# Performance work log

Measured on AMD Instinct MI355X. Metric: run time of the kernel, lower is better.

Reference implementation:

```python
import jax, jax.numpy as jnp
import numpy as np

N, E, F_IN, HID, H1, H2, H3, OUT = 10000, 160000, 50, 350, 4, 4, 6, 121


def _gat(x, src, dst, n, W, a_s, a_d, b, heads, C, concat):
    # PyG GATConv (dropout=0, eval): h = xW^T reshaped to [N,H,C]
    h = (x @ W.T).reshape(n, heads, C)
    alpha_src = jnp.einsum('nhc,hc->nh', h, a_s)  # [N,H]
    alpha_dst = jnp.einsum('nhc,hc->nh', h, a_d)  # [N,H]
    e = jax.nn.leaky_relu(alpha_src[src] + alpha_dst[dst], 0.2)  # [E,H]
    # numerically-stable segment softmax over incoming edges of each dst node
    m = jax.ops.segment_max(e, dst, num_segments=n)
    ee = jnp.exp(e - m[dst])
    s = jax.ops.segment_sum(ee, dst, num_segments=n)
    alpha = ee / s[dst]  # self-loops guarantee s > 0
    out = jax.ops.segment_sum(h[src] * alpha[:, :, None], dst, num_segments=n)  # [N,H,C]
    out = out.reshape(n, heads * C) if concat else out.mean(axis=1)
    return out + b


def setup_inputs() -> dict:
    key = jax.random.key(0)
    ks = jax.random.split(key, 16)
    sc = 0.05
    inp = {
        'x': jax.random.normal(ks[0], (N, F_IN), dtype=jnp.float32),
        'edge_index': jax.random.randint(ks[1], (2, E), 0, N, dtype=jnp.int64) if jax.config.jax_enable_x64 else jax.random.randint(ks[1], (2, E), 0, N, dtype=jnp.int32),
        'W1': jax.random.normal(ks[2], (H1 * HID, F_IN), dtype=jnp.float32) * sc,
        'a1s': jax.random.normal(ks[3], (H1, HID), dtype=jnp.float32) * sc,
        'a1d': jax.random.normal(ks[4], (H1, HID), dtype=jnp.float32) * sc,
        'b1': jnp.zeros((H1 * HID,), dtype=jnp.float32),
        'W2': jax.random.normal(ks[5], (H2 * HID, H1 * HID), dtype=jnp.float32) * sc,
        'a2s': jax.random.normal(ks[6], (H2, HID), dtype=jnp.float32) * sc,
        'a2d': jax.random.normal(ks[7], (H2, HID), dtype=jnp.float32) * sc,
        'b2': jnp.zeros((H2 * HID,), dtype=jnp.float32),
        'Wskip': jax.random.normal(ks[8], (H2 * HID, H1 * HID), dtype=jnp.float32) * sc,
        'W3': jax.random.normal(ks[9], (H3 * OUT, H2 * HID), dtype=jnp.float32) * sc,
        'a3s': jax.random.normal(ks[10], (H3, OUT), dtype=jnp.float32) * sc,
        'a3d': jax.random.normal(ks[11], (H3, OUT), dtype=jnp.float32) * sc,
        'b3': jnp.zeros((OUT,), dtype=jnp.float32),
    }
    return inp


def reference(x, edge_index, W1, a1s, a1d, b1, W2, a2s, a2d, b2, Wskip, W3, a3s, a3d, b3):
    n = x.shape[0]
    loops = jnp.arange(n, dtype=edge_index.dtype)  # PyG add_self_loops=True
    src = jnp.concatenate([edge_index[0], loops])
    dst = jnp.concatenate([edge_index[1], loops])
    h = jax.nn.elu(_gat(x, src, dst, n, W1, a1s, a1d, b1, H1, HID, True))
    x_in = h
    h = jax.nn.elu(_gat(h, src, dst, n, W2, a2s, a2d, b2, H2, HID, True))
    h = h + x_in @ Wskip.T  # skip connection (bias=False)
    return _gat(h, src, dst, n, W3, a3s, a3d, b3, H3, OUT, False)
```

## Files before the change

### kernel.cpp

```cpp
#include <hip/hip_runtime.h>
#include <math.h>

#define NNODES 10000
#define NEDGES 160000
#define E2 (NEDGES + NNODES)
#define F_IN 50
#define HIDC 350
#define NH1 4
#define NH2 4
#define NH3 6
#define OUTC 121
#define MAXE 96
#define KP1 64
#define KP2 1408
#define LD3 736
#define ROWSLACK 128

typedef __attribute__((ext_vector_type(8))) short short8;
typedef __attribute__((ext_vector_type(8))) unsigned short ushort8v;
typedef __attribute__((ext_vector_type(4))) float floatx4;

static __device__ __forceinline__ unsigned short f2bf(float f) {
    unsigned u = __float_as_uint(f);
    unsigned r = (u + 0x7fffu + ((u >> 16) & 1u)) >> 16;
    return (unsigned short)r;
}
static __device__ __forceinline__ float bf2f(unsigned short s) {
    return __uint_as_float(((unsigned)s) << 16);
}

#define GLL16(gp, lp)                                                      \
    __builtin_amdgcn_global_load_lds(                                      \
        (const __attribute__((address_space(1))) void*)(gp),               \
        (__attribute__((address_space(3))) void*)(lp), 16, 0, 0)

__global__ void count_kernel(const int* __restrict__ ei, int* __restrict__ cnt) {
    int i = blockIdx.x * blockDim.x + threadIdx.x;
    if (i >= E2) return;
    int dst = (i < NEDGES) ? ei[NEDGES + i] : (i - NEDGES);
    atomicAdd(&cnt[dst], 1);
}

__global__ void scan_kernel(const int* __restrict__ cnt, int* __restrict__ indptr,
                            int* __restrict__ cursor) {
    __shared__ int part[1024];
    int tid = threadIdx.x;
    const int CH = (NNODES + 1023) / 1024;
    int base = tid * CH;
    int s = 0;
    for (int i = 0; i < CH; i++) {
        int idx = base + i;
        if (idx < NNODES) s += cnt[idx];
    }
    part[tid] = s;
    __syncthreads();
    for (int off = 1; off < 1024; off <<= 1) {
        int v = (tid >= off) ? part[tid - off] : 0;
        __syncthreads();
        part[tid] += v;
        __syncthreads();
    }
    int run = (tid == 0) ? 0 : part[tid - 1];
    for (int i = 0; i < CH; i++) {
        int idx = base + i;
        if (idx < NNODES) {
            indptr[idx] = run;
            cursor[idx] = run;
            run += cnt[idx];
        }
    }
    if (tid == 0) indptr[NNODES] = part[1023];
}

__global__ void scatter_kernel(const int* __restrict__ ei, int* __restrict__ cursor,
                               int* __restrict__ esrc) {
    int i = blockIdx.x * blockDim.x + threadIdx.x;
    if (i >= E2) return;
    int src, dst;
    if (i < NEDGES) {
        src = ei[i];
        dst = ei[NEDGES + i];
    } else {
        src = dst = i - NEDGES;
    }
    int pos = atomicAdd(&cursor[dst], 1);
    esrc[pos] = src;
}

__global__ void splitW1_kernel(const float* __restrict__ W1,
                               unsigned short* __restrict__ w1Hi,
                               unsigned short* __restrict__ w1Lo) {
    int k = threadIdx.x;
    int r = blockIdx.x;
    float v = (k < F_IN) ? W1[(size_t)r * F_IN + k] : 0.f;
    unsigned short h = f2bf(v);
    w1Hi[(size_t)r * KP1 + k] = h;
    w1Lo[(size_t)r * KP1 + k] = f2bf(v - bf2f(h));
}

__global__ void splitB_kernel(const float* __restrict__ W2, const float* __restrict__ Wsk,
                              const float* __restrict__ W3,
                              unsigned short* __restrict__ w2Hi,
                              unsigned short* __restrict__ w3Hi) {
    int k = blockIdx.x * blockDim.x + threadIdx.x;
    if (k >= KP2) return;
    int r = blockIdx.y;
    const int K = 1400;
    const float* src;
    unsigned short* hi;
    int row;
    if (r < 1400) { src = W2; row = r; hi = w2Hi; }
    else if (r < 2800) { src = Wsk; row = r - 1400; hi = w2Hi + (size_t)1400 * KP2; }
    else { src = W3; row = r - 2800; hi = w3Hi; }
    float v = (k < K) ? src[(size_t)row * K + k] : 0.f;
    hi[(size_t)row * KP2 + k] = f2bf(v);
}

__global__ void atil_kernel(const float* __restrict__ W, const float* __restrict__ av_s,
                            const float* __restrict__ av_d, float* __restrict__ outS,
                            float* __restrict__ outD, int C, int K, int cchunk) {
    int k = blockIdx.x * 64 + (threadIdx.x & 63);
    if (k >= K) return;
    int h = blockIdx.y;
    int c0 = blockIdx.z * cchunk;
    int c1 = c0 + cchunk;
    if (c1 > C) c1 = C;
    float ss = 0.f, dd = 0.f;
    for (int c = c0; c < c1; c++) {
        float wv = W[((size_t)h * C + c) * K + k];
        ss = fmaf(wv, av_s[h * C + c], ss);
        dd = fmaf(wv, av_d[h * C + c], dd);
    }
    atomicAdd(&outS[(size_t)h * K + k], ss);
    atomicAdd(&outD[(size_t)h * K + k], dd);
}

__global__ __launch_bounds__(256) void alpha1x_kernel(const float* __restrict__ x,
                                                      const float* __restrict__ at1s,
                                                      const float* __restrict__ at1d,
                                                      float* __restrict__ as1,
                                                      float* __restrict__ ad1) {
    int wave = threadIdx.x >> 6, lane = threadIdx.x & 63;
    int n = blockIdx.x * 4 + wave;
    if (n >= NNODES) return;
    int kk = lane < F_IN ? lane : F_IN - 1;
    float v = (lane < F_IN) ? x[(size_t)n * F_IN + lane] : 0.f;
    float p[8];
#pragma unroll
    for (int h = 0; h < 4; h++) {
        p[h] = v * at1s[h * F_IN + kk];
        p[4 + h] = v * at1d[h * F_IN + kk];
    }
#pragma unroll
    for (int s = 0; s < 8; s++)
#pragma unroll
        for (int o = 32; o > 0; o >>= 1) p[s] += __shfl_xor(p[s], o, 64);
    if (lane == 0) {
#pragma unroll
        for (int h = 0; h < 4; h++) {
            as1[n * 4 + h] = p[h];
            ad1[n * 4 + h] = p[4 + h];
        }
    }
}

__global__ void zeropad_kernel(unsigned short* __restrict__ hi) {
    int i = blockIdx.x * 256 + threadIdx.x;
    if (i >= NNODES * 8) return;
    int n = i >> 3, c = 1400 + (i & 7);
    hi[(size_t)n * KP2 + c] = 0;
}

__global__ __launch_bounds__(256) void agg_x(
    const float* __restrict__ x, const float* __restrict__ as_n,
    const float* __restrict__ ad_n, const int* __restrict__ indptr,
    const int* __restrict__ esrc, unsigned short* __restrict__ xaggHi,
    unsigned short* __restrict__ xaggLo) {
    int n = blockIdx.x, tid = threadIdx.x;
    int s = indptr[n], e = indptr[n + 1];
    int deg = e - s;
    if (deg > MAXE) deg = MAXE;
    __shared__ int srcs[MAXE];
    __shared__ float wgt[MAXE * 4];

    if (tid < 64) {
        int lane = tid;
        float adv[4], mx[4], sm[4];
#pragma unroll
        for (int h = 0; h < 4; h++) {
            adv[h] = ad_n[n * 4 + h];
            mx[h] = -1e30f;
            sm[h] = 0.f;
        }
        for (int j = lane; j < deg; j += 64) {
            int sr = esrc[s + j];
            srcs[j] = sr;
#pragma unroll
            for (int h = 0; h < 4; h++) {
                float ev = as_n[sr * 4 + h] + adv[h];
                ev = ev > 0.f ? ev : 0.2f * ev;
                wgt[j * 4 + h] = ev;
                mx[h] = fmaxf(mx[h], ev);
            }
        }
#pragma unroll
        for (int h = 0; h < 4; h++)
#pragma unroll
            for (int o = 32; o > 0; o >>= 1) mx[h] = fmaxf(mx[h], __shfl_xor(mx[h], o, 64));
        for (int j = lane; j < deg; j += 64) {
#pragma unroll
            for (int h = 0; h < 4; h++) {
                float p = __expf(wgt[j * 4 + h] - mx[h]);
                wgt[j * 4 + h] = p;
                sm[h] += p;
            }
        }
#pragma unroll
        for (int h = 0; h < 4; h++) {
#pragma unroll
            for (int o = 32; o > 0; o >>= 1) sm[h] += __shfl_xor(sm[h], o, 64);
            sm[h] = 1.f / sm[h];
        }
        for (int j = lane; j < deg; j += 64) {
#pragma unroll
            for (int h = 0; h < 4; h++) wgt[j * 4 + h] *= sm[h];
        }
    }
    __syncthreads();

    int h = tid >> 6, k = tid & 63;
    float a = 0.f;
    if (k < F_IN) {
        float a2 = 0.f;
        int j = 0;
        for (; j + 1 < deg; j += 2) {
            a = fmaf(wgt[j * 4 + h], x[(size_t)srcs[j] * F_IN + k], a);
            a2 = fmaf(wgt[(j + 1) * 4 + h], x[(size_t)srcs[j + 1] * F_IN + k], a2);
        }
        if (j < deg) a = fmaf(wgt[j * 4 + h], x[(size_t)srcs[j] * F_IN + k], a);
        a += a2;
    }
    unsigned short hi = f2bf(a);
    xaggHi[(size_t)n * 256 + tid] = hi;
    xaggLo[(size_t)n * 256 + tid] = f2bf(a - bf2f(hi));
}

__global__ __launch_bounds__(256, 2) void gemm_h1(
    const unsigned short* __restrict__ xaggHi, const unsigned short* __restrict__ xaggLo,
    const unsigned short* __restrict__ w1Hi, const unsigned short* __restrict__ w1Lo,
    const float* __restrict__ bias, unsigned short* __restrict__ actHi) {
    __shared__ __align__(16) unsigned short sA[2][128 * 32];
    __shared__ __align__(16) unsigned short sB[2][256 * 32];
    int tid = threadIdx.x;
    int wave = tid >> 6, lane = tid & 63;
    int wm = (wave >> 1) * 64, wn = (wave & 1) * 128;
    int fr = lane & 15, kq = lane >> 4;
    int row0 = blockIdx.y * 128, col0 = blockIdx.x * 256;
    int hd = blockIdx.z;

    floatx4 acc[4][8];
#pragma unroll
    for (int i = 0; i < 4; i++)
#pragma unroll
        for (int j = 0; j < 8; j++)
#pragma unroll
            for (int q = 0; q < 4; q++) acc[i][j][q] = 0.f;

    int gpos = lane & 3;
    int rl = lane >> 2;
    int gsw = kq ^ ((fr >> 1) & 3);

    for (int k0 = 0; k0 < 64; k0 += 32) {
#pragma unroll
        for (int c = 0; c < 2; ++c) {
            int r = wave * 32 + c * 16 + rl;
            int g = gpos ^ ((r >> 1) & 3);
            size_t gofs = (size_t)(row0 + r) * 256 + hd * 64 + k0 + g * 8;
            size_t lofs = (size_t)r * 32 + (size_t)gpos * 8;
            GLL16(xaggHi + gofs, &sA[0][lofs]);
            GLL16(xaggLo + gofs, &sA[1][lofs]);
        }
#pragma unroll
        for (int c = 0; c < 4; ++c) {
            int r = wave * 64 + c * 16 + rl;
            int g = gpos ^ ((r >> 1) & 3);
            size_t gofs = (size_t)(hd * 350 + col0 + r) * KP1 + k0 + g * 8;
            size_t lofs = (size_t)r * 32 + (size_t)gpos * 8;
            GLL16(w1Hi + gofs, &sB[0][lofs]);
            GLL16(w1Lo + gofs, &sB[1][lofs]);
        }
        __syncthreads();

        short8 ah[4], al[4], bh[8], bl[8];
#pragma unroll
        for (int j = 0; j < 8; j++) {
            int rb = wn + j * 16 + fr;
            bh[j] = *(const short8*)&sB[0][rb * 32 + gsw * 8];
            bl[j] = *(const short8*)&sB[1][rb * 32 + gsw * 8];
        }
#pragma unroll
        for (int i = 0; i < 4; i++) {
            int ra = wm + i * 16 + fr;
            ah[i] = *(const short8*)&sA[0][ra * 32 + gsw * 8];
            al[i] = *(const short8*)&sA[1][ra * 32 + gsw * 8];
        }
#pragma unroll
        for (int i = 0; i < 4; i++)
#pragma unroll
            for (int j = 0; j < 8; j++) {
                acc[i][j] = __builtin_amdgcn_mfma_f32_16x16x32_bf16(ah[i], bh[j],
                                                                   acc[i][j], 0, 0, 0);
                acc[i][j] = __builtin_amdgcn_mfma_f32_16x16x32_bf16(al[i], bh[j],
                                                                   acc[i][j], 0, 0, 0);
                acc[i][j] = __builtin_amdgcn_mfma_f32_16x16x32_bf16(ah[i], bl[j],
                                                                   acc[i][j], 0, 0, 0);
            }
        __syncthreads();
    }

#pragma unroll
    for (int i = 0; i < 4; i++) {
#pragma unroll
        for (int rg = 0; rg < 4; rg++) {
            int rr = row0 + wm + i * 16 + kq * 4 + rg;
            if (rr >= NNODES) continue;
#pragma unroll
            for (int j = 0; j < 8; j++) {
                int cc = col0 + wn + j * 16 + fr;
                if (cc < 350) {
                    int gc = hd * 350 + cc;
                    float v = acc[i][j][rg] + bias[gc];
                    v = v > 0.f ? v : expm1f(v);
                    actHi[(size_t)rr * KP2 + gc] = f2bf(v);
                }
            }
        }
    }
}

__global__ __launch_bounds__(256) void alpha_act(
    const unsigned short* __restrict__ actHi, const float* __restrict__ ats,
    const float* __restrict__ atd, float* __restrict__ asx, float* __restrict__ adx) {
    int wave = threadIdx.x >> 6, lane = threadIdx.x & 63;
    int n = blockIdx.x * 4 + wave;
    if (n >= NNODES) return;
    float p[8] = {0.f, 0.f, 0.f, 0.f, 0.f, 0.f, 0.f, 0.f};
    for (int u = lane; u < 175; u += 64) {
        int cb = u * 8;
        const ushort8v v8 = *(const ushort8v*)(actHi + (size_t)n * KP2 + cb);
#pragma unroll
        for (int q = 0; q < 8; q++) {
            float v = bf2f(v8[q]);
#pragma unroll
            for (int h = 0; h < 4; h++) {
                p[h] = fmaf(v, ats[h * 1400 + cb + q], p[h]);
                p[4 + h] = fmaf(v, atd[h * 1400 + cb + q], p[4 + h]);
            }
        }
    }
#pragma unroll
    for (int q = 0; q < 8; q++)
#pragma unroll
        for (int o = 32; o > 0; o >>= 1) p[q] += __shfl_xor(p[q], o, 64);
    if (lane == 0) {
#pragma unroll
        for (int h = 0; h < 4; h++) {
            asx[n * 4 + h] = p[h];
            adx[n * 4 + h] = p[4 + h];
        }
    }
}

__global__ __launch_bounds__(256, 2) void gemm_b16(
    const unsigned short* __restrict__ A, const unsigned short* __restrict__ B,
    unsigned short* __restrict__ Cb, int NN, int M, int Kp, int ldc) {
    __shared__ __align__(16) unsigned short sA[128 * 32];
    __shared__ __align__(16) unsigned short sB[256 * 32];
    int tid = threadIdx.x;
    int wave = tid >> 6, lane = tid & 63;
    int wm = (wave >> 1) * 64, wn = (wave & 1) * 128;
    int fr = lane & 15, kq = lane >> 4;
    int row0 = blockIdx.y * 128, col0 = blockIdx.x * 256;

    floatx4 acc[4][8];
#pragma unroll
    for (int i = 0; i < 4; i++)
#pragma unroll
        for (int j = 0; j < 8; j++)
#pragma unroll
            for (int q = 0; q < 4; q++) acc[i][j][q] = 0.f;

    int gpos = lane & 3;
    int rl = lane >> 2;
    int gsw = kq ^ ((fr >> 1) & 3);

    for (int k0 = 0; k0 < Kp; k0 += 32) {
#pragma unroll
        for (int c = 0; c < 2; ++c) {
            int r = wave * 32 + c * 16 + rl;
            int g = gpos ^ ((r >> 1) & 3);
            GLL16(A + (size_t)(row0 + r) * Kp + k0 + g * 8,
                  &sA[(size_t)r * 32 + (size_t)gpos * 8]);
        }
#pragma unroll
        for (int c = 0; c < 4; ++c) {
            int r = wave * 64 + c * 16 + rl;
            int g = gpos ^ ((r >> 1) & 3);
            GLL16(B + (size_t)(col0 + r) * Kp + k0 + g * 8,
                  &sB[(size_t)r * 32 + (size_t)gpos * 8]);
        }
        __syncthreads();

        short8 ah[4], bh[8];
#pragma unroll
        for (int j = 0; j < 8; j++) {
            int rb = wn + j * 16 + fr;
            bh[j] = *(const short8*)&sB[rb * 32 + gsw * 8];
        }
#pragma unroll
        for (int i = 0; i < 4; i++) {
            int ra = wm + i * 16 + fr;
            ah[i] = *(const short8*)&sA[ra * 32 + gsw * 8];
        }
#pragma unroll
        for (int i = 0; i < 4; i++)
#pragma unroll
            for (int j = 0; j < 8; j++)
                acc[i][j] = __builtin_amdgcn_mfma_f32_16x16x32_bf16(ah[i], bh[j],
                                                                   acc[i][j], 0, 0, 0);
        __syncthreads();
    }

#pragma unroll
    for (int i = 0; i < 4; i++) {
#pragma unroll
        for (int rg = 0; rg < 4; rg++) {
            int rr = row0 + wm + i * 16 + kq * 4 + rg;
            if (rr >= NN) continue;
#pragma unroll
            for (int j = 0; j < 8; j++) {
                int cc = col0 + wn + j * 16 + fr;
                if (cc < M) Cb[(size_t)rr * ldc + cc] = f2bf(acc[i][j][rg]);
            }
        }
    }
}

#define AGG_T 192
template <int H, int C, int MODE, int DOELU, int SKIP, int HN>
__global__ __launch_bounds__(AGG_T) void agg2(
    const unsigned short* __restrict__ hpreb, int ldh,
    const float* __restrict__ as_n, const float* __restrict__ ad_n,
    const int* __restrict__ indptr, const int* __restrict__ esrc,
    const float* __restrict__ bias, unsigned short* __restrict__ outHi, int Kp,
    float* __restrict__ outF, const float* __restrict__ atns,
    const float* __restrict__ atnd, float* __restrict__ asx,
    float* __restrict__ adx) {
    constexpr int HC = H * C;
    int n = blockIdx.x;
    int tid = threadIdx.x;
    int s = indptr[n], e = indptr[n + 1];
    int deg = e - s;
    if (deg > MAXE) deg = MAXE;

    __shared__ int srcs[MAXE];
    __shared__ float wgt[MAXE * H];
    __shared__ float aggsh[MODE ? HC : 1];
    __shared__ float sAl[16];
    if (tid < 16) sAl[tid] = 0.f;

    if (tid < 64) {
        int lane = tid;
        float adv[H], mx[H], sm[H];
#pragma unroll
        for (int h = 0; h < H; h++) {
            adv[h] = ad_n[n * H + h];
            mx[h] = -1e30f;
            sm[h] = 0.f;
        }
        for (int j = lane; j < deg; j += 64) {
            int sr = esrc[s + j];
            srcs[j] = sr;
#pragma unroll
            for (int h = 0; h < H; h++) {
                float ev = as_n[sr * H + h] + adv[h];
                ev = ev > 0.f ? ev : 0.2f * ev;
                wgt[j * H + h] = ev;
                mx[h] = fmaxf(mx[h], ev);
            }
        }
#pragma unroll
        for (int h = 0; h < H; h++)
#pragma unroll
            for (int o = 32; o > 0; o >>= 1) mx[h] = fmaxf(mx[h], __shfl_xor(mx[h], o, 64));
        for (int j = lane; j < deg; j += 64) {
#pragma unroll
            for (int h = 0; h < H; h++) {
                float p = __expf(wgt[j * H + h] - mx[h]);
                wgt[j * H + h] = p;
                sm[h] += p;
            }
        }
#pragma unroll
        for (int h = 0; h < H; h++) {
#pragma unroll
            for (int o = 32; o > 0; o >>= 1) sm[h] += __shfl_xor(sm[h], o, 64);
            sm[h] = 1.f / sm[h];
        }
        for (int j = lane; j < deg; j += 64) {
#pragma unroll
            for (int h = 0; h < H; h++) wgt[j * H + h] *= sm[h];
        }
    }
    __syncthreads();

    if (MODE == 0) {
        constexpr int NV8 = HC / 8;
        constexpr int NP = (HN > 0) ? 2 * HN : 1;
        float p[NP];
#pragma unroll
        for (int q = 0; q < NP; q++) p[q] = 0.f;

        for (int c8 = tid; c8 < NV8; c8 += AGG_T) {
            int cb = c8 * 8;
            int hh[8];
#pragma unroll
            for (int q = 0; q < 8; q++) hh[q] = (cb + q) / C;
            float av[8];
#pragma unroll
            for (int q = 0; q < 8; q++) av[q] = 0.f;
            int j = 0;
            for (; j + 3 < deg; j += 4) {
                const ushort8v v0 = *(const ushort8v*)(hpreb + (size_t)srcs[j] * ldh + cb);
                const ushort8v v1 = *(const ushort8v*)(hpreb + (size_t)srcs[j + 1] * ldh + cb);
                const ushort8v v2 = *(const ushort8v*)(hpreb + (size_t)srcs[j + 2] * ldh + cb);
                const ushort8v v3 = *(const ushort8v*)(hpreb + (size_t)srcs[j + 3] * ldh + cb);
                const float* w0 = &wgt[j * H];
                const float* w1 = &wgt[(j + 1) * H];
                const float* w2 = &wgt[(j + 2) * H];
                const float* w3 = &wgt[(j + 3) * H];
#pragma unroll
                for (int q = 0; q < 8; q++) av[q] = fmaf(w0[hh[q]], bf2f(v0[q]), av[q]);
#pragma unroll
                for (int q = 0; q < 8; q++) av[q] = fmaf(w1[hh[q]], bf2f(v1[q]), av[q]);
#pragma unroll
                for (int q = 0; q < 8; q++) av[q] = fmaf(w2[hh[q]], bf2f(v2[q]), av[q]);
#pragma unroll
                for (int q = 0; q < 8; q++) av[q] = fmaf(w3[hh[q]], bf2f(v3[q]), av[q]);
            }
            for (; j < deg; j++) {
                const ushort8v v0 = *(const ushort8v*)(hpreb + (size_t)srcs[j] * ldh + cb);
                const float* w0 = &wgt[j * H];
#pragma unroll
                for (int q = 0; q < 8; q++) av[q] = fmaf(w0[hh[q]], bf2f(v0[q]), av[q]);
            }
#pragma unroll
            for (int q = 0; q < 8; q++) av[q] += bias[cb + q];
            if (DOELU) {
#pragma unroll
                for (int q = 0; q < 8; q++) av[q] = av[q] > 0.f ? av[q] : expm1f(av[q]);
            }
            if (SKIP) {
                const ushort8v sk = *(const ushort8v*)(hpreb + (size_t)n * ldh + 1400 + cb);
#pragma unroll
                for (int q = 0; q < 8; q++) av[q] += bf2f(sk[q]);
            }
            if (HN > 0) {
#pragma unroll
                for (int h = 0; h < HN; h++) {
                    float ss = 0.f, dd = 0.f;
#pragma unroll
                    for (int q = 0; q < 8; q++) {
                        ss = fmaf(av[q], atns[(size_t)h * HC + cb + q], ss);
                        dd = fmaf(av[q], atnd[(size_t)h * HC + cb + q], dd);
                    }
                    p[h] += ss;
                    p[HN + h] += dd;
                }
            }
            ushort8v hi8;
#pragma unroll
            for (int q = 0; q < 8; q++) hi8[q] = f2bf(av[q]);
            *(ushort8v*)(outHi + (size_t)n * Kp + cb) = hi8;
        }
        for (int c = HC + tid; c < Kp; c += AGG_T) outHi[(size_t)n * Kp + c] = 0;
        if (HN > 0) {
#pragma unroll
            for (int q = 0; q < NP; q++)
#pragma unroll
                for (int o = 32; o > 0; o >>= 1) p[q] += __shfl_xor(p[q], o, 64);
            if ((tid & 63) == 0) {
#pragma unroll
                for (int q = 0; q < NP; q++) atomicAdd(&sAl[q], p[q]);
            }
            __syncthreads();
            if (tid < HN) asx[n * HN + tid] = sAl[tid];
            else if (tid < 2 * HN) adx[n * HN + (tid - HN)] = sAl[tid];
        }
    } else {
        constexpr int NV8 = (HC + 7) / 8;
        for (int c8 = tid; c8 < NV8; c8 += AGG_T) {
            int cb = c8 * 8;
            int hh[8];
#pragma unroll
            for (int q = 0; q < 8; q++) {
                int cc = cb + q;
                hh[q] = (cc < HC) ? cc / C : (H - 1);
            }
            float av[8];
#pragma unroll
            for (int q = 0; q < 8; q++) av[q] = 0.f;
            int j = 0;
            for (; j + 3 < deg; j += 4) {
                const ushort8v v0 = *(const ushort8v*)(hpreb + (size_t)srcs[j] * ldh + cb);
                const ushort8v v1 = *(const ushort8v*)(hpreb + (size_t)srcs[j + 1] * ldh + cb);
                const ushort8v v2 = *(const ushort8v*)(hpreb + (size_t)srcs[j + 2] * ldh + cb);
                const ushort8v v3 = *(const ushort8v*)(hpreb + (size_t)srcs[j + 3] * ldh + cb);
                const float* w0 = &wgt[j * H];
                const float* w1 = &wgt[(j + 1) * H];
                const float* w2 = &wgt[(j + 2) * H];
                const float* w3 = &wgt[(j + 3) * H];
#pragma unroll
                for (int q = 0; q < 8; q++) av[q] = fmaf(w0[hh[q]], bf2f(v0[q]), av[q]);
#pragma unroll
                for (int q = 0; q < 8; q++) av[q] = fmaf(w1[hh[q]], bf2f(v1[q]), av[q]);
#pragma unroll
                for (int q = 0; q < 8; q++) av[q] = fmaf(w2[hh[q]], bf2f(v2[q]), av[q]);
#pragma unroll
                for (int q = 0; q < 8; q++) av[q] = fmaf(w3[hh[q]], bf2f(v3[q]), av[q]);
            }
            for (; j < deg; j++) {
                const ushort8v v0 = *(const ushort8v*)(hpreb + (size_t)srcs[j] * ldh + cb);
                const float* w0 = &wgt[j * H];
#pragma unroll
                for (int q = 0; q < 8; q++) av[q] = fmaf(w0[hh[q]], bf2f(v0[q]), av[q]);
            }
#pragma unroll
            for (int q = 0; q < 8; q++)
                if (cb + q < HC) aggsh[cb + q] = av[q];
        }
        __syncthreads();
        for (int c = tid; c < C; c += AGG_T) {
            float sres = 0.f;
#pragma unroll
            for (int h = 0; h < H; h++) sres += aggsh[h * C + c];
            outF[(size_t)n * C + c] = sres * (1.f / (float)H) + bias[c];
        }
    }
}

extern "C" void kernel_launch(void* const* d_in, const int* in_sizes, int n_in,
                              void* d_out, int out_size, void* d_ws, size_t ws_size,
                              hipStream_t stream) {
    const float* x = (const float*)d_in[0];
    const int* ei = (const int*)d_in[1];
    const float* W1 = (const float*)d_in[2];
    const float* a1s = (const float*)d_in[3];
    const float* a1d = (const float*)d_in[4];
    const float* b1 = (const float*)d_in[5];
    const float* W2 = (const float*)d_in[6];
    const float* a2s = (const float*)d_in[7];
    const float* a2d = (const float*)d_in[8];
    const float* b2 = (const float*)d_in[9];
    const float* Wsk = (const float*)d_in[10];
    const float* W3 = (const float*)d_in[11];
    const float* a3s = (const float*)d_in[12];
    const float* a3d = (const float*)d_in[13];
    const float* b3 = (const float*)d_in[14];
    float* out = (float*)d_out;

    char* w = (char*)d_ws;
    size_t off = 0;
    auto alloc = [&](size_t bytes) -> char* {
        char* p = w + off;
        off += (bytes + 255) & ~(size_t)255;
        return p;
    };
    unsigned short* hpreb = (unsigned short*)alloc((size_t)(NNODES + ROWSLACK) * 2800 * 2);
    unsigned short* actHi = (unsigned short*)alloc((size_t)(NNODES + ROWSLACK) * KP2 * 2);
    unsigned short* xaggHi = (unsigned short*)alloc((size_t)(NNODES + ROWSLACK) * 256 * 2);
    unsigned short* xaggLo = (unsigned short*)alloc((size_t)(NNODES + ROWSLACK) * 256 * 2);
    unsigned short* w1Hi = (unsigned short*)alloc((size_t)(1400 + 512) * KP1 * 2);
    unsigned short* w1Lo = (unsigned short*)alloc((size_t)(1400 + 512) * KP1 * 2);
    unsigned short* w2Hi = (unsigned short*)alloc((size_t)(2800 + ROWSLACK) * KP2 * 2);
    unsigned short* w3Hi = (unsigned short*)alloc((size_t)(726 + ROWSLACK) * KP2 * 2);
    float* atall = (float*)alloc((size_t)28400 * 4);
    int* cnt = (int*)alloc((size_t)(NNODES + 16) * 4);
    float* at1s = atall;
    float* at1d = atall + 200;
    float* at2s = atall + 400;
    float* at2d = atall + 6000;
    float* at3s = atall + 11600;
    float* at3d = atall + 20000;
    float* asP = (float*)alloc((size_t)NNODES * 6 * 4);
    float* adP = (float*)alloc((size_t)NNODES * 6 * 4);
    float* asQ = (float*)alloc((size_t)NNODES * 6 * 4);
    float* adQ = (float*)alloc((size_t)NNODES * 6 * 4);
    int* indptr = (int*)alloc((size_t)(NNODES + 16) * 4);
    int* cursor = (int*)alloc((size_t)(NNODES + 16) * 4);
    int* esrc = (int*)alloc((size_t)E2 * 4);

    size_t zbytes = (size_t)((char*)cnt - (char*)atall) + (NNODES + 16) * 4;
    hipMemsetAsync(atall, 0, zbytes, stream);

    splitW1_kernel<<<1400, 64, 0, stream>>>(W1, w1Hi, w1Lo);
    splitB_kernel<<<dim3(6, 2800 + 726), 256, 0, stream>>>(W2, Wsk, W3, w2Hi, w3Hi);
    atil_kernel<<<dim3(1, 4, 5), 64, 0, stream>>>(W1, a1s, a1d, at1s, at1d, HIDC, F_IN, 70);
    atil_kernel<<<dim3(22, 4, 5), 64, 0, stream>>>(W2, a2s, a2d, at2s, at2d, HIDC, 1400, 70);
    atil_kernel<<<dim3(22, 6, 4), 64, 0, stream>>>(W3, a3s, a3d, at3s, at3d, OUTC, 1400, 31);
    alpha1x_kernel<<<(NNODES + 3) / 4, 256, 0, stream>>>(x, at1s, at1d, asP, adP);

    count_kernel<<<(E2 + 255) / 256, 256, 0, stream>>>(ei, cnt);
    scan_kernel<<<1, 1024, 0, stream>>>(cnt, indptr, cursor);
    scatter_kernel<<<(E2 + 255) / 256, 256, 0, stream>>>(ei, cursor, esrc);

    zeropad_kernel<<<(NNODES * 8 + 255) / 256, 256, 0, stream>>>(actHi);

    dim3 blk(256);
    int gy = (NNODES + 127) / 128;

    agg_x<<<NNODES, 256, 0, stream>>>(x, asP, adP, indptr, esrc, xaggHi, xaggLo);
    gemm_h1<<<dim3(2, gy, 4), blk, 0, stream>>>(xaggHi, xaggLo, w1Hi, w1Lo, b1, actHi);
    alpha_act<<<(NNODES + 3) / 4, 256, 0, stream>>>(actHi, at2s, at2d, asQ, adQ);

    {
        int M = 2800;
        dim3 grid((M + 255) / 256, gy);
        gemm_b16<<<grid, blk, 0, stream>>>(actHi, w2Hi, hpreb, NNODES, M, KP2, 2800);
        agg2<NH2, HIDC, 0, 1, 1, 6><<<NNODES, AGG_T, 0, stream>>>(
            hpreb, 2800, asQ, adQ, indptr, esrc, b2, actHi, KP2, nullptr,
            at3s, at3d, asP, adP);
    }
    {
        int M = NH3 * OUTC;
        dim3 grid((M + 255) / 256, gy);
        gemm_b16<<<grid, blk, 0, stream>>>(actHi, w3Hi, hpreb, NNODES, M, KP2, LD3);
        agg2<NH3, OUTC, 1, 0, 0, 0><<<NNODES, AGG_T, 0, stream>>>(
            hpreb, LD3, asP, adP, indptr, esrc, b3, nullptr, 0, out,
            nullptr, nullptr, nullptr, nullptr);
    }
}
```

Before: 632.3 us.

## Compute layer-2 attention logits with MFMA and simplify head-weight selection in aggregation

Replaces the scalar per-node dot-product kernel that computes layer-2 attention logits with an MFMA kernel. Each wave handles 16 nodes against a 16-row bf16 hi/lo split of the folded attention vectors, and a new small kernel prepares that split. Separately, the aggregation kernels stop computing a per-element head index with integer division. Instead they pick between two preloaded per-edge weights based on a split point, which cuts LDS loads and divides in the inner edge loop. The MFMA path adds a setup kernel and relies on the padded activation columns being zero.

After: 635.1 us. No clear change (+0.4%).

```diff
diff --git a/kernel.cpp b/kernel.cpp
--- a/kernel.cpp
+++ b/kernel.cpp
@@ -135,6 +135,21 @@
     atomicAdd(&outD[(size_t)h * K + k], dd);
 }
 
+__global__ void splitAT2_kernel(const float* __restrict__ atall,
+                                unsigned short* __restrict__ atHi,
+                                unsigned short* __restrict__ atLo) {
+    int k = blockIdx.x * 64 + threadIdx.x;
+    int r = blockIdx.y;
+    float v = 0.f;
+    if (k < 1400) {
+        if (r < 4) v = atall[400 + r * 1400 + k];
+        else if (r < 8) v = atall[6000 + (r - 4) * 1400 + k];
+    }
+    unsigned short h = f2bf(v);
+    atHi[(size_t)r * KP2 + k] = h;
+    atLo[(size_t)r * KP2 + k] = f2bf(v - bf2f(h));
+}
+
 __global__ __launch_bounds__(256) void alpha1x_kernel(const float* __restrict__ x,
                                                       const float* __restrict__ at1s,
                                                       const float* __restrict__ at1d,
@@ -338,36 +353,31 @@
     }
 }
 
-__global__ __launch_bounds__(256) void alpha_act(
-    const unsigned short* __restrict__ actHi, const float* __restrict__ ats,
-    const float* __restrict__ atd, float* __restrict__ asx, float* __restrict__ adx) {
+__global__ __launch_bounds__(256) void alpha_mfma(
+    const unsigned short* __restrict__ act, const unsigned short* __restrict__ tHi,
+    const unsigned short* __restrict__ tLo, int H, float* __restrict__ asx,
+    float* __restrict__ adx) {
     int wave = threadIdx.x >> 6, lane = threadIdx.x & 63;
-    int n = blockIdx.x * 4 + wave;
-    if (n >= NNODES) return;
-    float p[8] = {0.f, 0.f, 0.f, 0.f, 0.f, 0.f, 0.f, 0.f};
-    for (int u = lane; u < 175; u += 64) {
-        int cb = u * 8;
-        const ushort8v v8 = *(const ushort8v*)(actHi + (size_t)n * KP2 + cb);
-#pragma unroll
-        for (int q = 0; q < 8; q++) {
-            float v = bf2f(v8[q]);
-#pragma unroll
-            for (int h = 0; h < 4; h++) {
-                p[h] = fmaf(v, ats[h * 1400 + cb + q], p[h]);
-                p[4 + h] = fmaf(v, atd[h * 1400 + cb + q], p[4 + h]);
-            }
-        }
-    }
-#pragma unroll
-    for (int q = 0; q < 8; q++)
-#pragma unroll
-        for (int o = 32; o > 0; o >>= 1) p[q] += __shfl_xor(p[q], o, 64);
-    if (lane == 0) {
-#pragma unroll
-        for (int h = 0; h < 4; h++) {
-            asx[n * 4 + h] = p[h];
-            adx[n * 4 + h] = p[4 + h];
-        }
+    int row0 = (blockIdx.x * 4 + wave) * 16;
+    if (row0 >= NNODES) return;
+    int fr = lane & 15, kq = lane >> 4;
+    floatx4 acc = {0.f, 0.f, 0.f, 0.f};
+    const unsigned short* arow = act + (size_t)(row0 + fr) * KP2 + kq * 8;
+    const unsigned short* brh = tHi + (size_t)fr * KP2 + kq * 8;
+    const unsigned short* brl = tLo + (size_t)fr * KP2 + kq * 8;
+#pragma unroll 4
+    for (int k0 = 0; k0 < KP2; k0 += 32) {
+        short8 a = *(const short8*)(arow + k0);
+        short8 vh = *(const short8*)(brh + k0);
+        short8 vl = *(const short8*)(brl + k0);
+        acc = __builtin_amdgcn_mfma_f32_16x16x32_bf16(a, vh, acc, 0, 0, 0);
+        acc = __builtin_amdgcn_mfma_f32_16x16x32_bf16(a, vl, acc, 0, 0, 0);
+    }
+#pragma unroll
+    for (int rg = 0; rg < 4; rg++) {
+        int rr = row0 + kq * 4 + rg;
+        if (fr < H) asx[rr * H + fr] = acc[rg];
+        else if (fr < 2 * H) adx[rr * H + (fr - H)] = acc[rg];
     }
 }
 
@@ -523,9 +533,10 @@
 
         for (int c8 = tid; c8 < NV8; c8 += AGG_T) {
             int cb = c8 * 8;
-            int hh[8];
-#pragma unroll
-            for (int q = 0; q < 8; q++) hh[q] = (cb + q) / C;
+            int h0 = cb / C;
+            int sp = (h0 + 1) * C - cb;
+            if (sp > 8) sp = 8;
+            int h1 = (h0 + 1 < H) ? h0 + 1 : h0;
             float av[8];
 #pragma unroll
             for (int q = 0; q < 8; q++) av[q] = 0.f;
@@ -535,24 +546,24 @@
                 const ushort8v v1 = *(const ushort8v*)(hpreb + (size_t)srcs[j + 1] * ldh + cb);
                 const ushort8v v2 = *(const ushort8v*)(hpreb + (size_t)srcs[j + 2] * ldh + cb);
                 const ushort8v v3 = *(const ushort8v*)(hpreb + (size_t)srcs[j + 3] * ldh + cb);
-                const float* w0 = &wgt[j * H];
-                const float* w1 = &wgt[(j + 1) * H];
-                const float* w2 = &wgt[(j + 2) * H];
-                const float* w3 = &wgt[(j + 3) * H];
-#pragma unroll
-                for (int q = 0; q < 8; q++) av[q] = fmaf(w0[hh[q]], bf2f(v0[q]), av[q]);
-#pragma unroll
-                for (int q = 0; q < 8; q++) av[q] = fmaf(w1[hh[q]], bf2f(v1[q]), av[q]);
-#pragma unroll
-                for (int q = 0; q < 8; q++) av[q] = fmaf(w2[hh[q]], bf2f(v2[q]), av[q]);
-#pragma unroll
-                for (int q = 0; q < 8; q++) av[q] = fmaf(w3[hh[q]], bf2f(v3[q]), av[q]);
+                float wa0 = wgt[j * H + h0], wa1 = wgt[j * H + h1];
+                float wb0 = wgt[(j + 1) * H + h0], wb1 = wgt[(j + 1) * H + h1];
+                float wc0 = wgt[(j + 2) * H + h0], wc1 = wgt[(j + 2) * H + h1];
+                float wd0 = wgt[(j + 3) * H + h0], wd1 = wgt[(j + 3) * H + h1];
+#pragma unroll
+                for (int q = 0; q < 8; q++) av[q] = fmaf(q < sp ? wa0 : wa1, bf2f(v0[q]), av[q]);
+#pragma unroll
+                for (int q = 0; q < 8; q++) av[q] = fmaf(q < sp ? wb0 : wb1, bf2f(v1[q]), av[q]);
+#pragma unroll
+                for (int q = 0; q < 8; q++) av[q] = fmaf(q < sp ? wc0 : wc1, bf2f(v2[q]), av[q]);
+#pragma unroll
+                for (int q = 0; q < 8; q++) av[q] = fmaf(q < sp ? wd0 : wd1, bf2f(v3[q]), av[q]);
             }
             for (; j < deg; j++) {
                 const ushort8v v0 = *(const ushort8v*)(hpreb + (size_t)srcs[j] * ldh + cb);
-                const float* w0 = &wgt[j * H];
-#pragma unroll
-                for (int q = 0; q < 8; q++) av[q] = fmaf(w0[hh[q]], bf2f(v0[q]), av[q]);
+                float wa0 = wgt[j * H + h0], wa1 = wgt[j * H + h1];
+#pragma unroll
+                for (int q = 0; q < 8; q++) av[q] = fmaf(q < sp ? wa0 : wa1, bf2f(v0[q]), av[q]);
             }
 #pragma unroll
             for (int q = 0; q < 8; q++) av[q] += bias[cb + q];
@@ -601,12 +612,11 @@
         constexpr int NV8 = (HC + 7) / 8;
         for (int c8 = tid; c8 < NV8; c8 += AGG_T) {
             int cb = c8 * 8;
-            int hh[8];
-#pragma unroll
-            for (int q = 0; q < 8; q++) {
-                int cc = cb + q;
-                hh[q] = (cc < HC) ? cc / C : (H - 1);
-            }
+            int h0 = cb / C;
+            if (h0 >= H) h0 = H - 1;
+            int sp = (h0 + 1) * C - cb;
+            if (sp > 8) sp = 8;
+            int h1 = (h0 + 1 < H) ? h0 + 1 : h0;
             float av[8];
 #pragma unroll
             for (int q = 0; q < 8; q++) av[q] = 0.f;
@@ -616,24 +626,24 @@
                 const ushort8v v1 = *(const ushort8v*)(hpreb + (size_t)srcs[j + 1] * ldh + cb);
                 const ushort8v v2 = *(const ushort8v*)(hpreb + (size_t)srcs[j + 2] * ldh + cb);
                 const ushort8v v3 = *(const ushort8v*)(hpreb + (size_t)srcs[j + 3] * ldh + cb);
-                const float* w0 = &wgt[j * H];
-                const float* w1 = &wgt[(j + 1) * H];
-                const float* w2 = &wgt[(j + 2) * H];
-                const float* w3 = &wgt[(j + 3) * H];
-#pragma unroll
-                for (int q = 0; q < 8; q++) av[q] = fmaf(w0[hh[q]], bf2f(v0[q]), av[q]);
-#pragma unroll
-                for (int q = 0; q < 8; q++) av[q] = fmaf(w1[hh[q]], bf2f(v1[q]), av[q]);
-#pragma unroll
-                for (int q = 0; q < 8; q++) av[q] = fmaf(w2[hh[q]], bf2f(v2[q]), av[q]);
-#pragma unroll
-                for (int q = 0; q < 8; q++) av[q] = fmaf(w3[hh[q]], bf2f(v3[q]), av[q]);
+                float wa0 = wgt[j * H + h0], wa1 = wgt[j * H + h1];
+                float wb0 = wgt[(j + 1) * H + h0], wb1 = wgt[(j + 1) * H + h1];
+                float wc0 = wgt[(j + 2) * H + h0], wc1 = wgt[(j + 2) * H + h1];
+                float wd0 = wgt[(j + 3) * H + h0], wd1 = wgt[(j + 3) * H + h1];
+#pragma unroll
+                for (int q = 0; q < 8; q++) av[q] = fmaf(q < sp ? wa0 : wa1, bf2f(v0[q]), av[q]);
+#pragma unroll
+                for (int q = 0; q < 8; q++) av[q] = fmaf(q < sp ? wb0 : wb1, bf2f(v1[q]), av[q]);
+#pragma unroll
+                for (int q = 0; q < 8; q++) av[q] = fmaf(q < sp ? wc0 : wc1, bf2f(v2[q]), av[q]);
+#pragma unroll
+                for (int q = 0; q < 8; q++) av[q] = fmaf(q < sp ? wd0 : wd1, bf2f(v3[q]), av[q]);
             }
             for (; j < deg; j++) {
                 const ushort8v v0 = *(const ushort8v*)(hpreb + (size_t)srcs[j] * ldh + cb);
-                const float* w0 = &wgt[j * H];
-#pragma unroll
-                for (int q = 0; q < 8; q++) av[q] = fmaf(w0[hh[q]], bf2f(v0[q]), av[q]);
+                float wa0 = wgt[j * H + h0], wa1 = wgt[j * H + h1];
+#pragma unroll
+                for (int q = 0; q < 8; q++) av[q] = fmaf(q < sp ? wa0 : wa1, bf2f(v0[q]), av[q]);
             }
 #pragma unroll
             for (int q = 0; q < 8; q++)
@@ -684,6 +694,8 @@
     unsigned short* w1Lo = (unsigned short*)alloc((size_t)(1400 + 512) * KP1 * 2);
     unsigned short* w2Hi = (unsigned short*)alloc((size_t)(2800 + ROWSLACK) * KP2 * 2);
     unsigned short* w3Hi = (unsigned short*)alloc((size_t)(726 + ROWSLACK) * KP2 * 2);
+    unsigned short* at2Hi = (unsigned short*)alloc((size_t)16 * KP2 * 2);
+    unsigned short* at2Lo = (unsigned short*)alloc((size_t)16 * KP2 * 2);
     float* atall = (float*)alloc((size_t)28400 * 4);
     int* cnt = (int*)alloc((size_t)(NNODES + 16) * 4);
     float* at1s = atall;
@@ -708,6 +720,7 @@
     atil_kernel<<<dim3(1, 4, 5), 64, 0, stream>>>(W1, a1s, a1d, at1s, at1d, HIDC, F_IN, 70);
     atil_kernel<<<dim3(22, 4, 5), 64, 0, stream>>>(W2, a2s, a2d, at2s, at2d, HIDC, 1400, 70);
     atil_kernel<<<dim3(22, 6, 4), 64, 0, stream>>>(W3, a3s, a3d, at3s, at3d, OUTC, 1400, 31);
+    splitAT2_kernel<<<dim3(22, 16), 64, 0, stream>>>(atall, at2Hi, at2Lo);
     alpha1x_kernel<<<(NNODES + 3) / 4, 256, 0, stream>>>(x, at1s, at1d, asP, adP);
 
     count_kernel<<<(E2 + 255) / 256, 256, 0, stream>>>(ei, cnt);
@@ -721,7 +734,7 @@
 
     agg_x<<<NNODES, 256, 0, stream>>>(x, asP, adP, indptr, esrc, xaggHi, xaggLo);
     gemm_h1<<<dim3(2, gy, 4), blk, 0, stream>>>(xaggHi, xaggLo, w1Hi, w1Lo, b1, actHi);
-    alpha_act<<<(NNODES + 3) / 4, 256, 0, stream>>>(actHi, at2s, at2d, asQ, adQ);
+    alpha_mfma<<<(NNODES / 16 + 3) / 4, 256, 0, stream>>>(actHi, at2Hi, at2Lo, 4, asQ, adQ);
 
     {
         int M = 2800;
```
